# Optimization experiments

Hardware: AMD Instinct MI355X
Metric: run time of the kernel (lower is better)

## Reference

```python
import jax, jax.numpy as jnp
import numpy as np

EMBED_DIM = 256
NUM_HEADS = 8
HEAD_DIM = EMBED_DIM // NUM_HEADS
LN_EPS = 1e-5


def _linear_init(key, fan_in, fan_out):
    # torch nn.Linear default: U(-1/sqrt(fan_in), 1/sqrt(fan_in)) for W and b
    kw, kb = jax.random.split(key)
    bound = 1.0 / np.sqrt(fan_in)
    W = jax.random.uniform(kw, (fan_out, fan_in), jnp.float32, -bound, bound)
    b = jax.random.uniform(kb, (fan_out,), jnp.float32, -bound, bound)
    return W, b


def setup_inputs() -> dict:
    key = jax.random.key(0)
    ks = jax.random.split(key, 6)
    x = jax.random.normal(ks[0], (2, 512, EMBED_DIM), jnp.float32)
    Wq, bq = _linear_init(ks[1], EMBED_DIM, EMBED_DIM)
    Wk, bk = _linear_init(ks[2], EMBED_DIM, EMBED_DIM)
    Wv, bv = _linear_init(ks[3], EMBED_DIM, EMBED_DIM)
    Wr, br = _linear_init(ks[4], EMBED_DIM, EMBED_DIM)
    Wo, bo = _linear_init(ks[5], EMBED_DIM, EMBED_DIM)
    g1 = jnp.ones((EMBED_DIM,), jnp.float32)
    b1 = jnp.zeros((EMBED_DIM,), jnp.float32)
    g2 = jnp.ones((EMBED_DIM,), jnp.float32)
    b2 = jnp.zeros((EMBED_DIM,), jnp.float32)
    return {"x": x, "Wq": Wq, "bq": bq, "Wk": Wk, "bk": bk, "Wv": Wv, "bv": bv,
            "Wr": Wr, "br": br, "Wo": Wo, "bo": bo,
            "g1": g1, "b1": b1, "g2": g2, "b2": b2}


def _layer_norm(x, g, b):
    mu = jnp.mean(x, axis=-1, keepdims=True)
    var = jnp.mean(jnp.square(x - mu), axis=-1, keepdims=True)
    return (x - mu) * jax.lax.rsqrt(var + LN_EPS) * g + b


def reference(x, Wq, bq, Wk, bk, Wv, bv, Wr, br, Wo, bo, g1, b1, g2, b2):
    B, N, D = x.shape
    H, Dh = NUM_HEADS, HEAD_DIM
    Q = x @ Wq.T + bq  # [B,N,D]
    K = x @ Wk.T + bk
    V = x @ Wv.T + bv
    # pairwise differences, projected: [B,N,N,D]
    R = x[:, :, None, :] - x[:, None, :, :]
    R = jnp.einsum('bijd,ed->bije', R, Wr) + br
    max_R1 = jnp.max(R, axis=1)  # [B,N,D] (max over rows -> bias for Q)
    max_R2 = jnp.max(R, axis=2)  # [B,N,D] (max over cols -> bias for K)
    Q_r = Q + max_R1
    K_r = K + max_R2
    # [B,H,N,Dh]
    Q_r = Q_r.reshape(B, N, H, Dh).transpose(0, 2, 1, 3)
    K_r = K_r.reshape(B, N, H, Dh).transpose(0, 2, 1, 3)
    Vh = V.reshape(B, N, H, Dh).transpose(0, 2, 1, 3)
    scores = jnp.einsum('bhqd,bhkd->bhqk', Q_r, K_r) / np.sqrt(Dh).astype(np.float32)
    probs = jax.nn.softmax(scores, axis=-1)
    attn = jnp.einsum('bhqk,bhkd->bhqd', probs, Vh)
    attn = attn.transpose(0, 2, 1, 3).reshape(B, N, D)
    attn = attn @ Wo.T + bo  # dropout is identity in eval mode
    h = _layer_norm(x + attn, g1, b1)
    return _layer_norm(h, g2, b2)
```

## Files before the change

kernel.cpp:

```cpp
#include <hip/hip_runtime.h>
#include <hip/hip_bf16.h>
#include <math.h>

#define NSEQ 512
#define EMB 256

typedef __attribute__((ext_vector_type(8))) short bf16x8;
typedef __attribute__((ext_vector_type(4))) float f32x4;

__device__ __forceinline__ unsigned short f2bf(float f) {
    unsigned u = __float_as_uint(f);
    unsigned r = (u + 0x7FFFu + ((u >> 16) & 1u)) >> 16;
    return (unsigned short)r;
}
__device__ __forceinline__ float bf2f(unsigned short s) {
    return __uint_as_float(((unsigned)s) << 16);
}
__device__ __forceinline__ ushort4 cvt4(float4 v) {
    ushort4 o;
    o.x = f2bf(v.x); o.y = f2bf(v.y); o.z = f2bf(v.z); o.w = f2bf(v.w);
    return o;
}

__global__ __launch_bounds__(256) void k_gemm_mfma(
    const float* __restrict__ X,
    const float* __restrict__ Wq, const float* __restrict__ Wk,
    const float* __restrict__ Wv, const float* __restrict__ Wr,
    const float* __restrict__ Wo,
    const float* __restrict__ bq, const float* __restrict__ bv,
    unsigned short* __restrict__ Qb, unsigned short* __restrict__ Kb,
    unsigned short* __restrict__ Vtb, unsigned short* __restrict__ Wob,
    float* __restrict__ maxPart)
{
    const int t = threadIdx.x;

    if (blockIdx.y == 16) {
        const float4* Wg = (const float4*)Wo;
        #pragma unroll
        for (int i = 0; i < 4; ++i) {
            int idx4 = blockIdx.x * 1024 + i * 256 + t;
            ((ushort4*)Wob)[idx4] = cvt4(Wg[idx4]);
        }
        return;
    }

    __shared__ __align__(16) unsigned short Xs[64 * 264];
    __shared__ __align__(16) unsigned short Ws[64 * 264];
    __shared__ float red[4][64];

    const int w = t >> 6, l = t & 63;
    const int ln = l & 15, kg = l >> 4;
    const int m0 = blockIdx.x * 64;
    const int nW = blockIdx.y * 64;
    const int seg = blockIdx.y >> 2;
    const int wbase = (blockIdx.y & 3) * 64;

    const float4* X4  = (const float4*)X;
    const float4* Wq4 = (const float4*)Wq;
    const float4* Wk4 = (const float4*)Wk;
    const float4* Wv4 = (const float4*)Wv;
    const float4* Wr4 = (const float4*)Wr;

    #pragma unroll
    for (int i = 0; i < 16; ++i) {
        int idx = i * 256 + t;
        int row = idx >> 6, c4 = idx & 63;
        float4 xv = X4[(size_t)(m0 + row) * 64 + c4];
        *(ushort4*)(Xs + row * 264 + c4 * 4) = cvt4(xv);

        size_t off = (size_t)(wbase + row) * 64 + c4;
        float4 wv;
        if (seg == 0) {
            float4 a = Wq4[off], r = Wr4[off];
            wv = make_float4(a.x - r.x, a.y - r.y, a.z - r.z, a.w - r.w);
        } else if (seg == 1) {
            float4 a = Wk4[off], r = Wr4[off];
            wv = make_float4(a.x + r.x, a.y + r.y, a.z + r.z, a.w + r.w);
        } else if (seg == 2) {
            wv = Wv4[off];
        } else {
            wv = Wr4[off];
        }
        *(ushort4*)(Ws + row * 264 + c4 * 4) = cvt4(wv);
    }
    __syncthreads();

    f32x4 acc[4] = {{0.f,0.f,0.f,0.f},{0.f,0.f,0.f,0.f},
                    {0.f,0.f,0.f,0.f},{0.f,0.f,0.f,0.f}};
    const int arow = (w << 4) + ln;
    #pragma unroll
    for (int ks = 0; ks < 8; ++ks) {
        bf16x8 a = *(const bf16x8*)(Xs + arow * 264 + ks * 32 + kg * 8);
        #pragma unroll
        for (int nf = 0; nf < 4; ++nf) {
            bf16x8 b = *(const bf16x8*)(Ws + (nf * 16 + ln) * 264 + ks * 32 + kg * 8);
            acc[nf] = __builtin_amdgcn_mfma_f32_16x16x32_bf16(a, b, acc[nf], 0, 0, 0);
        }
    }

    if (seg == 0) {
        #pragma unroll
        for (int nf = 0; nf < 4; ++nf) {
            int c = (nW & 255) + nf * 16 + ln;
            float bb = bq[c];
            #pragma unroll
            for (int r = 0; r < 4; ++r) {
                int row = m0 + w * 16 + kg * 4 + r;
                Qb[(size_t)row * 256 + c] = f2bf(acc[nf][r] + bb);
            }
        }
    } else if (seg == 1) {
        #pragma unroll
        for (int nf = 0; nf < 4; ++nf) {
            int c = (nW & 255) + nf * 16 + ln;
            #pragma unroll
            for (int r = 0; r < 4; ++r) {
                int row = m0 + w * 16 + kg * 4 + r;
                Kb[(size_t)row * 256 + c] = f2bf(acc[nf][r]);
            }
        }
    } else if (seg == 2) {
        #pragma unroll
        for (int nf = 0; nf < 4; ++nf) {
            int c = (nW & 255) + nf * 16 + ln;
            int h = c >> 5, d = c & 31;
            float bb = bv[c];
            #pragma unroll
            for (int r = 0; r < 4; ++r) {
                int row = m0 + w * 16 + kg * 4 + r;
                int b = row >> 9, ml = row & 511;
                Vtb[((size_t)(b * 8 + h) * 32 + d) * 512 + ml] = f2bf(acc[nf][r] + bb);
            }
        }
    } else {
        #pragma unroll
        for (int nf = 0; nf < 4; ++nf) {
            float mx = fmaxf(fmaxf(acc[nf][0], acc[nf][1]),
                             fmaxf(acc[nf][2], acc[nf][3]));
            mx = fmaxf(mx, __shfl_xor(mx, 16));
            mx = fmaxf(mx, __shfl_xor(mx, 32));
            if (l < 16) red[w][nf * 16 + ln] = mx;
        }
        __syncthreads();
        if (t < 64) {
            float m = fmaxf(fmaxf(red[0][t], red[1][t]),
                            fmaxf(red[2][t], red[3][t]));
            const int b = blockIdx.x >> 3;
            const int mblk = blockIdx.x & 7;
            maxPart[b * 2048 + mblk * 256 + (nW & 255) + t] = m;
        }
    }
}

__global__ __launch_bounds__(256) void k_attn_mfma(
    const unsigned short* __restrict__ Qb,
    const unsigned short* __restrict__ Kb,
    const unsigned short* __restrict__ Vtb,
    const float* __restrict__ maxPart,
    const float* __restrict__ br,
    unsigned short* __restrict__ attnb)
{
    __shared__ __align__(16) unsigned short Plds[4][32][136];
    __shared__ float Olds[4][32][33];
    __shared__ float mlds[4][32], llds[4][32];
    __shared__ float scl[4][32], Li[32];
    __shared__ float qadd[32];

    const int t = threadIdx.x;
    const int w = t >> 6, l = t & 63;
    const int ln = l & 15, kg = l >> 4;
    const int q0 = blockIdx.x * 32;
    const int h = blockIdx.y, bz = blockIdx.z;
    const int e0 = h * 32;
    const int bh = bz * 8 + h;
    const float scale = 0.17677669529663687f;

    if (t < 32) {
        float m = maxPart[bz * 2048 + e0 + t];
        #pragma unroll
        for (int j = 1; j < 8; ++j)
            m = fmaxf(m, maxPart[bz * 2048 + j * 256 + e0 + t]);
        qadd[t] = m + br[e0 + t];
    }
    __syncthreads();

    bf16x8 af[2];
    #pragma unroll
    for (int qf = 0; qf < 2; ++qf) {
        size_t qrow = (size_t)(bz * NSEQ + q0 + qf * 16 + ln) * 256 + e0 + kg * 8;
        bf16x8 qa = *(const bf16x8*)(Qb + qrow);
        #pragma unroll
        for (int j = 0; j < 8; ++j) {
            int d = kg * 8 + j;
            af[qf][j] = (short)f2bf((bf2f((unsigned short)qa[j]) + qadd[d]) * scale);
        }
    }

    const int key0 = w * 128;
    f32x4 sc[2][8];
    #pragma unroll
    for (int kf = 0; kf < 8; ++kf) {
        size_t krow = (size_t)(bz * NSEQ + key0 + kf * 16 + ln) * 256 + e0 + kg * 8;
        bf16x8 bfr = *(const bf16x8*)(Kb + krow);
        f32x4 z = {0.f, 0.f, 0.f, 0.f};
        sc[0][kf] = __builtin_amdgcn_mfma_f32_16x16x32_bf16(af[0], bfr, z, 0, 0, 0);
        sc[1][kf] = __builtin_amdgcn_mfma_f32_16x16x32_bf16(af[1], bfr, z, 0, 0, 0);
    }

    float m_[2][4], l_[2][4];
    #pragma unroll
    for (int qf = 0; qf < 2; ++qf) {
        #pragma unroll
        for (int r = 0; r < 4; ++r) {
            float mx = sc[qf][0][r];
            #pragma unroll
            for (int kf = 1; kf < 8; ++kf) mx = fmaxf(mx, sc[qf][kf][r]);
            #pragma unroll
            for (int off = 1; off < 16; off <<= 1) mx = fmaxf(mx, __shfl_xor(mx, off));
            m_[qf][r] = mx;
            float s = 0.f;
            #pragma unroll
            for (int kf = 0; kf < 8; ++kf) {
                float p = __expf(sc[qf][kf][r] - mx);
                sc[qf][kf][r] = p;
                s += p;
            }
            #pragma unroll
            for (int off = 1; off < 16; off <<= 1) s += __shfl_xor(s, off);
            l_[qf][r] = s;
        }
    }

    #pragma unroll
    for (int qf = 0; qf < 2; ++qf)
        #pragma unroll
        for (int kf = 0; kf < 8; ++kf)
            #pragma unroll
            for (int r = 0; r < 4; ++r)
                Plds[w][qf * 16 + kg * 4 + r][kf * 16 + ln] = f2bf(sc[qf][kf][r]);

    f32x4 o[2][2] = {{{0.f,0.f,0.f,0.f},{0.f,0.f,0.f,0.f}},
                     {{0.f,0.f,0.f,0.f},{0.f,0.f,0.f,0.f}}};
    #pragma unroll
    for (int ks = 0; ks < 4; ++ks) {
        bf16x8 vf[2];
        #pragma unroll
        for (int df = 0; df < 2; ++df) {
            size_t vrow = ((size_t)bh * 32 + df * 16 + ln) * 512 + key0 + ks * 32 + kg * 8;
            vf[df] = *(const bf16x8*)(Vtb + vrow);
        }
        #pragma unroll
        for (int qf = 0; qf < 2; ++qf) {
            bf16x8 pf = *(const bf16x8*)&Plds[w][qf * 16 + ln][ks * 32 + kg * 8];
            o[qf][0] = __builtin_amdgcn_mfma_f32_16x16x32_bf16(pf, vf[0], o[qf][0], 0, 0, 0);
            o[qf][1] = __builtin_amdgcn_mfma_f32_16x16x32_bf16(pf, vf[1], o[qf][1], 0, 0, 0);
        }
    }

    if (ln == 0) {
        #pragma unroll
        for (int qf = 0; qf < 2; ++qf)
            #pragma unroll
            for (int r = 0; r < 4; ++r) {
                mlds[w][qf * 16 + kg * 4 + r] = m_[qf][r];
                llds[w][qf * 16 + kg * 4 + r] = l_[qf][r];
            }
    }
    #pragma unroll
    for (int qf = 0; qf < 2; ++qf)
        #pragma unroll
        for (int df = 0; df < 2; ++df)
            #pragma unroll
            for (int r = 0; r < 4; ++r)
                Olds[w][qf * 16 + kg * 4 + r][df * 16 + ln] = o[qf][df][r];
    __syncthreads();

    if (t < 32) {
        float M = fmaxf(fmaxf(mlds[0][t], mlds[1][t]),
                        fmaxf(mlds[2][t], mlds[3][t]));
        float L = 0.f;
        #pragma unroll
        for (int wv = 0; wv < 4; ++wv) {
            float s = __expf(mlds[wv][t] - M);
            scl[wv][t] = s;
            L += s * llds[wv][t];
        }
        Li[t] = 1.f / L;
    }
    __syncthreads();

    #pragma unroll
    for (int i = 0; i < 4; ++i) {
        int idx = t + 256 * i;
        int q = idx >> 5, d = idx & 31;
        float acc = 0.f;
        #pragma unroll
        for (int wv = 0; wv < 4; ++wv)
            acc += scl[wv][q] * Olds[wv][q][d];
        attnb[(size_t)(bz * NSEQ + q0 + q) * 256 + e0 + d] = f2bf(acc * Li[q]);
    }
}

__global__ __launch_bounds__(256) void k_ogemm_mfma(
    const unsigned short* __restrict__ Ab,
    const unsigned short* __restrict__ Wob,
    unsigned short* __restrict__ yPb)
{
    __shared__ __align__(16) unsigned short As_[64 * 72];
    __shared__ __align__(16) unsigned short Bs_[64 * 72];

    const int t = threadIdx.x;
    const int w = t >> 6, l = t & 63;
    const int ln = l & 15, kg = l >> 4;
    const int m0 = blockIdx.x * 64;
    const int n0 = blockIdx.y * 64;
    const int bz = blockIdx.z;

    const uint4* Ag = (const uint4*)Ab;
    const uint4* Wg = (const uint4*)Wob;
    #pragma unroll
    for (int i = 0; i < 2; ++i) {
        int idx = i * 256 + t;
        int row = idx >> 3, c8 = idx & 7;
        *(uint4*)(As_ + row * 72 + c8 * 8) = Ag[(size_t)(m0 + row) * 32 + bz * 8 + c8];
        *(uint4*)(Bs_ + row * 72 + c8 * 8) = Wg[(size_t)(n0 + row) * 32 + bz * 8 + c8];
    }
    __syncthreads();

    f32x4 acc[4] = {{0.f,0.f,0.f,0.f},{0.f,0.f,0.f,0.f},
                    {0.f,0.f,0.f,0.f},{0.f,0.f,0.f,0.f}};
    const int arow = (w << 4) + ln;
    #pragma unroll
    for (int ks = 0; ks < 2; ++ks) {
        bf16x8 a = *(const bf16x8*)(As_ + arow * 72 + ks * 32 + kg * 8);
        #pragma unroll
        for (int nf = 0; nf < 4; ++nf) {
            bf16x8 b = *(const bf16x8*)(Bs_ + (nf * 16 + ln) * 72 + ks * 32 + kg * 8);
            acc[nf] = __builtin_amdgcn_mfma_f32_16x16x32_bf16(a, b, acc[nf], 0, 0, 0);
        }
    }

    unsigned short* dst = yPb + (size_t)bz * (1024 * 256);
    #pragma unroll
    for (int nf = 0; nf < 4; ++nf) {
        #pragma unroll
        for (int r = 0; r < 4; ++r) {
            int row = m0 + w * 16 + kg * 4 + r;
            dst[(size_t)row * 256 + n0 + nf * 16 + ln] = f2bf(acc[nf][r]);
        }
    }
}

__global__ __launch_bounds__(256) void k_lnorm(
    const unsigned short* __restrict__ yPb, const float* __restrict__ x,
    const float* __restrict__ bo,
    const float* __restrict__ g1, const float* __restrict__ b1,
    const float* __restrict__ g2, const float* __restrict__ b2,
    float* __restrict__ out)
{
    __shared__ float red[4][4][2];
    const int t = threadIdx.x;
    const int r0 = blockIdx.x * 4;
    const int c = t;
    const int wid = t >> 6, lane = t & 63;

    float y[4];
    #pragma unroll
    for (int r = 0; r < 4; ++r) {
        size_t off = (size_t)(r0 + r) * 256 + c;
        y[r] = x[off] + bo[c]
             + bf2f(yPb[off]) + bf2f(yPb[262144 + off])
             + bf2f(yPb[524288 + off]) + bf2f(yPb[786432 + off]);
    }

    #pragma unroll
    for (int r = 0; r < 4; ++r) {
        float s = y[r], s2 = y[r] * y[r];
        #pragma unroll
        for (int off = 32; off > 0; off >>= 1) {
            s  += __shfl_xor(s, off);
            s2 += __shfl_xor(s2, off);
        }
        if (lane == 0) { red[wid][r][0] = s; red[wid][r][1] = s2; }
    }
    __syncthreads();
    float t1[4];
    #pragma unroll
    for (int r = 0; r < 4; ++r) {
        float s  = red[0][r][0] + red[1][r][0] + red[2][r][0] + red[3][r][0];
        float s2 = red[0][r][1] + red[1][r][1] + red[2][r][1] + red[3][r][1];
        float mu = s * (1.f / 256.f);
        float var = s2 * (1.f / 256.f) - mu * mu;
        float rs = rsqrtf(var + 1e-5f);
        t1[r] = (y[r] - mu) * rs * g1[c] + b1[c];
    }
    __syncthreads();

    #pragma unroll
    for (int r = 0; r < 4; ++r) {
        float s = t1[r], s2 = t1[r] * t1[r];
        #pragma unroll
        for (int off = 32; off > 0; off >>= 1) {
            s  += __shfl_xor(s, off);
            s2 += __shfl_xor(s2, off);
        }
        if (lane == 0) { red[wid][r][0] = s; red[wid][r][1] = s2; }
    }
    __syncthreads();
    #pragma unroll
    for (int r = 0; r < 4; ++r) {
        float s  = red[0][r][0] + red[1][r][0] + red[2][r][0] + red[3][r][0];
        float s2 = red[0][r][1] + red[1][r][1] + red[2][r][1] + red[3][r][1];
        float mu = s * (1.f / 256.f);
        float var = s2 * (1.f / 256.f) - mu * mu;
        float rs = rsqrtf(var + 1e-5f);
        out[(size_t)(r0 + r) * 256 + c] = (t1[r] - mu) * rs * g2[c] + b2[c];
    }
}

extern "C" void kernel_launch(void* const* d_in, const int* in_sizes, int n_in,
                              void* d_out, int out_size, void* d_ws, size_t ws_size,
                              hipStream_t stream)
{
    const float* x  = (const float*)d_in[0];
    const float* Wq = (const float*)d_in[1];
    const float* bq = (const float*)d_in[2];
    const float* Wk = (const float*)d_in[3];
    const float* bk = (const float*)d_in[4];
    const float* Wv = (const float*)d_in[5];
    const float* bv = (const float*)d_in[6];
    const float* Wr = (const float*)d_in[7];
    const float* br = (const float*)d_in[8];
    const float* Wo = (const float*)d_in[9];
    const float* bo = (const float*)d_in[10];
    const float* g1 = (const float*)d_in[11];
    const float* b1 = (const float*)d_in[12];
    const float* g2 = (const float*)d_in[13];
    const float* b2 = (const float*)d_in[14];
    float* out = (float*)d_out;
    (void)bk;

    unsigned short* u = (unsigned short*)d_ws;
    unsigned short* Qb    = u;
    unsigned short* Kb    = u + 262144;
    unsigned short* Vtb   = u + 524288;
    unsigned short* attnb = u + 786432;
    unsigned short* Wob   = u + 1048576;
    float* maxPart = (float*)(u + 1114112);
    unsigned short* yPb = u + 1122304;

    k_gemm_mfma<<<dim3(16, 17), 256, 0, stream>>>(x, Wq, Wk, Wv, Wr, Wo, bq, bv,
                                                  Qb, Kb, Vtb, Wob, maxPart);
    k_attn_mfma<<<dim3(16, 8, 2), 256, 0, stream>>>(Qb, Kb, Vtb, maxPart, br, attnb);
    k_ogemm_mfma<<<dim3(16, 4, 4), 256, 0, stream>>>(attnb, Wob, yPb);
    k_lnorm<<<256, 256, 0, stream>>>(yPb, x, bo, g1, b1, g2, b2, out);
}
```

Before: 27.10 us.

## Fuse output projection into attention kernel with per-head partial sums

The attention kernel now keeps its normalized per-head output in shared memory and immediately multiplies it by the head's 32-column slice of Wo using MFMA. It writes 8 per-head bf16 partial products that the layernorm kernel sums. This removes the separate output-GEMM launch and the attn buffer round trip. In exchange, the partial-sum traffic doubles from 4 to 8 bf16 slices, and Wo fragments are read straight from global memory without LDS staging.

After: 27.28 us. Within noise of the previous version (+0.7%).

```diff
diff --git a/kernel.cpp b/kernel.cpp
--- a/kernel.cpp
+++ b/kernel.cpp
@@ -152,19 +152,21 @@
     }
 }
 
-__global__ __launch_bounds__(256) void k_attn_mfma(
+__global__ __launch_bounds__(256) void k_attn_og(
     const unsigned short* __restrict__ Qb,
     const unsigned short* __restrict__ Kb,
     const unsigned short* __restrict__ Vtb,
+    const unsigned short* __restrict__ Wob,
     const float* __restrict__ maxPart,
     const float* __restrict__ br,
-    unsigned short* __restrict__ attnb)
+    unsigned short* __restrict__ yPh)
 {
     __shared__ __align__(16) unsigned short Plds[4][32][136];
     __shared__ float Olds[4][32][33];
     __shared__ float mlds[4][32], llds[4][32];
     __shared__ float scl[4][32], Li[32];
     __shared__ float qadd[32];
+    __shared__ __align__(16) unsigned short Ob[32][36];
 
     const int t = threadIdx.x;
     const int w = t >> 6, l = t & 63;
@@ -297,62 +299,34 @@
         #pragma unroll
         for (int wv = 0; wv < 4; ++wv)
             acc += scl[wv][q] * Olds[wv][q][d];
-        attnb[(size_t)(bz * NSEQ + q0 + q) * 256 + e0 + d] = f2bf(acc * Li[q]);
-    }
-}
-
-__global__ __launch_bounds__(256) void k_ogemm_mfma(
-    const unsigned short* __restrict__ Ab,
-    const unsigned short* __restrict__ Wob,
-    unsigned short* __restrict__ yPb)
-{
-    __shared__ __align__(16) unsigned short As_[64 * 72];
-    __shared__ __align__(16) unsigned short Bs_[64 * 72];
-
-    const int t = threadIdx.x;
-    const int w = t >> 6, l = t & 63;
-    const int ln = l & 15, kg = l >> 4;
-    const int m0 = blockIdx.x * 64;
-    const int n0 = blockIdx.y * 64;
-    const int bz = blockIdx.z;
-
-    const uint4* Ag = (const uint4*)Ab;
-    const uint4* Wg = (const uint4*)Wob;
-    #pragma unroll
-    for (int i = 0; i < 2; ++i) {
-        int idx = i * 256 + t;
-        int row = idx >> 3, c8 = idx & 7;
-        *(uint4*)(As_ + row * 72 + c8 * 8) = Ag[(size_t)(m0 + row) * 32 + bz * 8 + c8];
-        *(uint4*)(Bs_ + row * 72 + c8 * 8) = Wg[(size_t)(n0 + row) * 32 + bz * 8 + c8];
-    }
-    __syncthreads();
-
-    f32x4 acc[4] = {{0.f,0.f,0.f,0.f},{0.f,0.f,0.f,0.f},
-                    {0.f,0.f,0.f,0.f},{0.f,0.f,0.f,0.f}};
-    const int arow = (w << 4) + ln;
-    #pragma unroll
-    for (int ks = 0; ks < 2; ++ks) {
-        bf16x8 a = *(const bf16x8*)(As_ + arow * 72 + ks * 32 + kg * 8);
-        #pragma unroll
-        for (int nf = 0; nf < 4; ++nf) {
-            bf16x8 b = *(const bf16x8*)(Bs_ + (nf * 16 + ln) * 72 + ks * 32 + kg * 8);
-            acc[nf] = __builtin_amdgcn_mfma_f32_16x16x32_bf16(a, b, acc[nf], 0, 0, 0);
-        }
-    }
-
-    unsigned short* dst = yPb + (size_t)bz * (1024 * 256);
+        Ob[q][d] = f2bf(acc * Li[q]);
+    }
+    __syncthreads();
+
+    bf16x8 aog[2];
+    #pragma unroll
+    for (int qf = 0; qf < 2; ++qf)
+        aog[qf] = *(const bf16x8*)&Ob[qf * 16 + ln][kg * 8];
+
+    unsigned short* dst = yPh + (size_t)h * (1024 * 256);
     #pragma unroll
     for (int nf = 0; nf < 4; ++nf) {
+        int n = w * 64 + nf * 16 + ln;
+        bf16x8 bfr = *(const bf16x8*)(Wob + (size_t)n * 256 + e0 + kg * 8);
+        f32x4 z = {0.f, 0.f, 0.f, 0.f};
+        f32x4 y0 = __builtin_amdgcn_mfma_f32_16x16x32_bf16(aog[0], bfr, z, 0, 0, 0);
+        f32x4 y1 = __builtin_amdgcn_mfma_f32_16x16x32_bf16(aog[1], bfr, z, 0, 0, 0);
         #pragma unroll
         for (int r = 0; r < 4; ++r) {
-            int row = m0 + w * 16 + kg * 4 + r;
-            dst[(size_t)row * 256 + n0 + nf * 16 + ln] = f2bf(acc[nf][r]);
+            size_t row0 = (size_t)(bz * NSEQ + q0 + kg * 4 + r);
+            dst[row0 * 256 + n] = f2bf(y0[r]);
+            dst[(row0 + 16) * 256 + n] = f2bf(y1[r]);
         }
     }
 }
 
 __global__ __launch_bounds__(256) void k_lnorm(
-    const unsigned short* __restrict__ yPb, const float* __restrict__ x,
+    const unsigned short* __restrict__ yPh, const float* __restrict__ x,
     const float* __restrict__ bo,
     const float* __restrict__ g1, const float* __restrict__ b1,
     const float* __restrict__ g2, const float* __restrict__ b2,
@@ -368,9 +342,11 @@
     #pragma unroll
     for (int r = 0; r < 4; ++r) {
         size_t off = (size_t)(r0 + r) * 256 + c;
-        y[r] = x[off] + bo[c]
-             + bf2f(yPb[off]) + bf2f(yPb[262144 + off])
-             + bf2f(yPb[524288 + off]) + bf2f(yPb[786432 + off]);
+        float acc = x[off] + bo[c];
+        #pragma unroll
+        for (int h = 0; h < 8; ++h)
+            acc += bf2f(yPh[(size_t)h * 262144 + off]);
+        y[r] = acc;
     }
 
     #pragma unroll
@@ -441,17 +417,16 @@
     (void)bk;
 
     unsigned short* u = (unsigned short*)d_ws;
-    unsigned short* Qb    = u;
-    unsigned short* Kb    = u + 262144;
-    unsigned short* Vtb   = u + 524288;
-    unsigned short* attnb = u + 786432;
-    unsigned short* Wob   = u + 1048576;
-    float* maxPart = (float*)(u + 1114112);
-    unsigned short* yPb = u + 1122304;
+    unsigned short* Qb   = u;
+    unsigned short* Kb   = u + 262144;
+    unsigned short* Vtb  = u + 524288;
+    unsigned short* Wob  = u + 786432;
+    float* maxPart = (float*)(u + 851968);
+    unsigned short* yPh = u + 860160;
 
     k_gemm_mfma<<<dim3(16, 17), 256, 0, stream>>>(x, Wq, Wk, Wv, Wr, Wo, bq, bv,
                                                   Qb, Kb, Vtb, Wob, maxPart);
-    k_attn_mfma<<<dim3(16, 8, 2), 256, 0, stream>>>(Qb, Kb, Vtb, maxPart, br, attnb);
-    k_ogemm_mfma<<<dim3(16, 4, 4), 256, 0, stream>>>(attnb, Wob, yPb);
-    k_lnorm<<<256, 256, 0, stream>>>(yPb, x, bo, g1, b1, g2, b2, out);
-}
+    k_attn_og<<<dim3(16, 8, 2), 256, 0, stream>>>(Qb, Kb, Vtb, Wob, maxPart,
+                                                  br, yPh);
+    k_lnorm<<<256, 256, 0, stream>>>(yPh, x, bo, g1, b1, g2, b2, out);
+}
```
